# Kernel tuning notes

Measured on AMD Instinct MI355X. Metric: run time of the kernel, lower is better.

## Reference

```python
import jax, jax.numpy as jnp
import numpy as np

# NaiveMatryoshkaLinear(dim=4096, hidden_dim=4096, heads=[8,8,16], bias=False)
# head_dim = 4096 // 32 = 128
# input_dims  (cumsum heads * head_dim) = [1024, 2048, 4096]
# output_dims (heads * head_dim)        = [1024, 1024, 2048]
INPUT_DIMS = (1024, 2048, 4096)
OUTPUT_DIMS = (1024, 1024, 2048)


def setup_inputs() -> dict:
    key = jax.random.key(0)
    kx, k0, k1, k2 = jax.random.split(key, 4)
    x = jax.random.normal(kx, (4, 4096, 4096), dtype=jnp.float32)
    # torch nn.Linear weight layout: (out_features, in_features), kaiming-uniform-ish init
    def init_w(k, out_d, in_d):
        bound = 1.0 / np.sqrt(in_d)
        return jax.random.uniform(k, (out_d, in_d), dtype=jnp.float32, minval=-bound, maxval=bound)
    W0 = init_w(k0, OUTPUT_DIMS[0], INPUT_DIMS[0])
    W1 = init_w(k1, OUTPUT_DIMS[1], INPUT_DIMS[1])
    W2 = init_w(k2, OUTPUT_DIMS[2], INPUT_DIMS[2])
    return {"x": x, "W0": W0, "W1": W1, "W2": W2}


def reference(x, W0, W1, W2):
    # Block-triangular matryoshka linear: each head i projects the prefix
    # x[..., :input_dims[i]] with its own weight, outputs are concatenated.
    y0 = jnp.einsum('bsd,od->bso', x[..., :INPUT_DIMS[0]], W0)
    y1 = jnp.einsum('bsd,od->bso', x[..., :INPUT_DIMS[1]], W1)
    y2 = jnp.einsum('bsd,od->bso', x[..., :INPUT_DIMS[2]], W2)
    return jnp.concatenate([y0, y1, y2], axis=-1)  # [4, 4096, 4096]
```

## Files before the change

### kernel.cpp

```cpp
#include <hip/hip_runtime.h>
#include <hip/hip_bf16.h>


typedef short bf16x8 __attribute__((ext_vector_type(8)));
typedef float f32x4 __attribute__((ext_vector_type(4)));

__device__ __forceinline__ ushort f2bf(float f) {
  union { float f; unsigned u; } c; c.f = f;
  unsigned u = c.u;
  unsigned r = u + 0x7fffu + ((u >> 16) & 1u);
  return (ushort)(r >> 16);
}

__global__ void cvt_all_bf16(const float* __restrict__ x,
                             const float* __restrict__ W0,
                             const float* __restrict__ W1,
                             const float* __restrict__ W2,
                             ushort* __restrict__ dst) {
  const int X4  = 16777216;
  const int E0  = X4 + 262144;
  const int E1  = E0 + 524288;
  const int E2  = E1 + 2097152;
  int i = blockIdx.x * blockDim.x + threadIdx.x;
  int stride = gridDim.x * blockDim.x;
  ushort4* out4 = (ushort4*)dst;
  for (int j = i; j < E2; j += stride) {
    const float4* src;
    if (j < X4)      src = (const float4*)x  + j;
    else if (j < E0) src = (const float4*)W0 + (j - X4);
    else if (j < E1) src = (const float4*)W1 + (j - E0);
    else             src = (const float4*)W2 + (j - E1);
    float4 v = *src;
    ushort4 o;
    o.x = f2bf(v.x); o.y = f2bf(v.y); o.z = f2bf(v.z); o.w = f2bf(v.w);
    out4[j] = o;
  }
}

__device__ __forceinline__ void gload16(const ushort* g, const ushort* l) {
  __builtin_amdgcn_global_load_lds(
      (const __attribute__((address_space(1))) void*)g,
      (__attribute__((address_space(3))) void*)l, 16, 0, 0);
}

#define TILE_E 8192

#define MF(av, bv, mi, ni) \
  acc[mi][ni] = __builtin_amdgcn_mfma_f32_16x16x32_bf16(av, bv, acc[mi][ni], 0, 0, 0)

__global__ __launch_bounds__(512, 2) void matry_gemm(
    const ushort* __restrict__ xbf,
    const ushort* __restrict__ w0,
    const ushort* __restrict__ w1,
    const ushort* __restrict__ w2,
    float* __restrict__ out) {
  __shared__ __align__(16) ushort sA[4][TILE_E];
  __shared__ __align__(16) ushort sB[4][TILE_E];

  const int bid = blockIdx.x;
  const int rt = bid & 63;
  const int ct = bid >> 6;

  int K; const ushort* W; int nl0;
  if (ct < 4)      { K = 1024; W = w0; nl0 = ct * 256; }
  else if (ct < 8) { K = 2048; W = w1; nl0 = (ct - 4) * 256; }
  else             { K = 4096; W = w2; nl0 = (ct - 8) * 256; }
  const int NT = K >> 5;
  const int m0 = rt * 256;
  const int n0 = ct * 256;

  const int tid  = threadIdx.x;
  const int wid  = tid >> 6;
  const int lane = tid & 63;
  const int wm = wid >> 2;
  const int wn = wid & 3;
  const int fr = lane & 15;
  const int swz_e = (((lane >> 4) ^ ((lane >> 1) & 3)) << 3);

  const int srow = tid >> 2;
  const int scol = (((tid & 3) ^ ((tid >> 3) & 3)) << 3);
  const ushort* Asrc0 = xbf + (size_t)(m0 + srow) * 4096 + scol;
  const ushort* Asrc1 = Asrc0 + (size_t)128 * 4096;
  const ushort* Bsrc0 = W + (size_t)(nl0 + srow) * K + scol;
  const ushort* Bsrc1 = Bsrc0 + (size_t)128 * K;
  const int d0 = tid * 8;
  const int d1 = 4096 + tid * 8;

  f32x4 acc[8][4];
#pragma unroll
  for (int mi = 0; mi < 8; ++mi)
#pragma unroll
    for (int ni = 0; ni < 4; ++ni)
      acc[mi][ni] = (f32x4){0.f, 0.f, 0.f, 0.f};

#pragma unroll
  for (int pt = 0; pt < 3; ++pt) {
    const int ks = pt * 32;
    gload16(Asrc0 + ks, &sA[pt][d0]);
    gload16(Asrc1 + ks, &sA[pt][d1]);
    gload16(Bsrc0 + ks, &sB[pt][d0]);
    gload16(Bsrc1 + ks, &sB[pt][d1]);
  }
  asm volatile("s_waitcnt vmcnt(8)" ::: "memory");
  __builtin_amdgcn_s_barrier();

  for (int t = 0; t < NT; ++t) {
    const int b = t & 3;
    const ushort* pa = &sA[b][(wm * 128 + fr) * 32 + swz_e];
    const ushort* pb = &sB[b][(wn * 64 + fr) * 32 + swz_e];
    const int ts = (t + 3 < NT) ? (t + 3) : (NT - 1);
    const int ks = ts << 5;
    const int bs = (t + 3) & 3;

    bf16x8 a0 = *(const bf16x8*)(pa);
    bf16x8 a1 = *(const bf16x8*)(pa + 512);
    bf16x8 a2 = *(const bf16x8*)(pa + 1024);
    bf16x8 a3 = *(const bf16x8*)(pa + 1536);
    bf16x8 b0 = *(const bf16x8*)(pb);
    bf16x8 b1 = *(const bf16x8*)(pb + 512);
    bf16x8 b2 = *(const bf16x8*)(pb + 1024);
    bf16x8 b3 = *(const bf16x8*)(pb + 1536);
    gload16(Asrc0 + ks, &sA[bs][d0]);
    gload16(Asrc1 + ks, &sA[bs][d1]);
    __builtin_amdgcn_s_barrier();
    asm volatile("s_waitcnt lgkmcnt(0)" ::: "memory");
    __builtin_amdgcn_s_setprio(1);
    MF(a0, b0, 0, 0); MF(a0, b1, 0, 1); MF(a0, b2, 0, 2); MF(a0, b3, 0, 3);
    MF(a1, b0, 1, 0); MF(a1, b1, 1, 1); MF(a1, b2, 1, 2); MF(a1, b3, 1, 3);
    MF(a2, b0, 2, 0); MF(a2, b1, 2, 1); MF(a2, b2, 2, 2); MF(a2, b3, 2, 3);
    MF(a3, b0, 3, 0); MF(a3, b1, 3, 1); MF(a3, b2, 3, 2); MF(a3, b3, 3, 3);
    __builtin_amdgcn_s_setprio(0);
    __builtin_amdgcn_s_barrier();

    bf16x8 a4 = *(const bf16x8*)(pa + 2048);
    bf16x8 a5 = *(const bf16x8*)(pa + 2560);
    bf16x8 a6 = *(const bf16x8*)(pa + 3072);
    bf16x8 a7 = *(const bf16x8*)(pa + 3584);
    gload16(Bsrc0 + ks, &sB[bs][d0]);
    gload16(Bsrc1 + ks, &sB[bs][d1]);
    __builtin_amdgcn_s_barrier();
    asm volatile("s_waitcnt lgkmcnt(0)" ::: "memory");
    __builtin_amdgcn_s_setprio(1);
    MF(a4, b0, 4, 0); MF(a4, b1, 4, 1); MF(a4, b2, 4, 2); MF(a4, b3, 4, 3);
    MF(a5, b0, 5, 0); MF(a5, b1, 5, 1); MF(a5, b2, 5, 2); MF(a5, b3, 5, 3);
    MF(a6, b0, 6, 0); MF(a6, b1, 6, 1); MF(a6, b2, 6, 2); MF(a6, b3, 6, 3);
    MF(a7, b0, 7, 0); MF(a7, b1, 7, 1); MF(a7, b2, 7, 2); MF(a7, b3, 7, 3);
    __builtin_amdgcn_s_setprio(0);
    asm volatile("s_waitcnt vmcnt(8)" ::: "memory");
    __builtin_amdgcn_s_barrier();
  }

  const int rq = (lane >> 4) * 4;
#pragma unroll
  for (int mi = 0; mi < 8; ++mi) {
#pragma unroll
    for (int ni = 0; ni < 4; ++ni) {
      const int n = n0 + wn * 64 + ni * 16 + fr;
#pragma unroll
      for (int r = 0; r < 4; ++r) {
        const int m = m0 + wm * 128 + mi * 16 + rq + r;
        out[(size_t)m * 4096 + n] = acc[mi][ni][r];
      }
    }
  }
}

__global__ void naive_kernel(const float* __restrict__ x,
                             const float* __restrict__ W0,
                             const float* __restrict__ W1,
                             const float* __restrict__ W2,
                             float* __restrict__ out) {
  long idx = (long)blockIdx.x * 256 + threadIdx.x;
  int n = (int)(idx & 4095);
  long m = idx >> 12;
  int K; const float* W; int nl;
  if (n < 1024)      { K = 1024; W = W0; nl = n; }
  else if (n < 2048) { K = 2048; W = W1; nl = n - 1024; }
  else               { K = 4096; W = W2; nl = n - 2048; }
  const float* xr = x + m * 4096;
  const float* wr = W + (long)nl * K;
  float s = 0.f;
  for (int k = 0; k < K; ++k) s += xr[k] * wr[k];
  out[idx] = s;
}

extern "C" void kernel_launch(void* const* d_in, const int* in_sizes, int n_in,
                              void* d_out, int out_size, void* d_ws,
                              size_t ws_size, hipStream_t stream) {
  const float* x  = (const float*)d_in[0];
  const float* W0 = (const float*)d_in[1];
  const float* W1 = (const float*)d_in[2];
  const float* W2 = (const float*)d_in[3];
  float* out = (float*)d_out;

  const size_t xN  = (size_t)16384 * 4096;
  const size_t w0N = (size_t)1024 * 1024;
  const size_t w1N = (size_t)1024 * 2048;
  const size_t w2N = (size_t)2048 * 4096;
  const size_t need = (xN + w0N + w1N + w2N) * sizeof(ushort);

  if (ws_size >= need) {
    ushort* xbf = (ushort*)d_ws;
    ushort* w0b = xbf + xN;
    ushort* w1b = w0b + w0N;
    ushort* w2b = w1b + w1N;
    cvt_all_bf16<<<4096, 256, 0, stream>>>(x, W0, W1, W2, xbf);
    matry_gemm<<<1024, 512, 0, stream>>>(xbf, w0b, w1b, w2b, out);
  } else {
    naive_kernel<<<(int)((xN + 255) / 256), 256, 0, stream>>>(x, W0, W1, W2, out);
  }
}
```

Before: 478.5 us.

## Restructure GEMM main loop to double-buffered 64-wide K steps with half-tile buffers

Replaces the four-deep ring of 32-wide K tiles with two double-buffered halves (sA0/sA1, sB0/sB1), so each loop iteration processes 64 of K in four MFMA phases. Prefetch distance drops from three tiles to the next 64-wide step, and register reuse is tightened by recycling the a/b fragment variables. The intent is less loop overhead and bookkeeping per MFMA while keeping LDS usage the same. In exchange the prefetch is shallower, which may expose more global-load latency, and the vmcnt accounting changes.

New measurement: 563.9 us. 1.18x slower.

```diff
diff --git a/kernel.cpp b/kernel.cpp
--- a/kernel.cpp
+++ b/kernel.cpp
@@ -43,10 +43,20 @@
       (__attribute__((address_space(3))) void*)l, 16, 0, 0);
 }
 
-#define TILE_E 8192
-
 #define MF(av, bv, mi, ni) \
   acc[mi][ni] = __builtin_amdgcn_mfma_f32_16x16x32_bf16(av, bv, acc[mi][ni], 0, 0, 0)
+
+#define MFQ0(A0, A1, A2, A3) \
+  MF(A0, b0, 0, 0); MF(A0, b1, 0, 1); MF(A0, b2, 0, 2); MF(A0, b3, 0, 3); \
+  MF(A1, b0, 1, 0); MF(A1, b1, 1, 1); MF(A1, b2, 1, 2); MF(A1, b3, 1, 3); \
+  MF(A2, b0, 2, 0); MF(A2, b1, 2, 1); MF(A2, b2, 2, 2); MF(A2, b3, 2, 3); \
+  MF(A3, b0, 3, 0); MF(A3, b1, 3, 1); MF(A3, b2, 3, 2); MF(A3, b3, 3, 3)
+
+#define MFQ1(A0, A1, A2, A3) \
+  MF(A0, b0, 4, 0); MF(A0, b1, 4, 1); MF(A0, b2, 4, 2); MF(A0, b3, 4, 3); \
+  MF(A1, b0, 5, 0); MF(A1, b1, 5, 1); MF(A1, b2, 5, 2); MF(A1, b3, 5, 3); \
+  MF(A2, b0, 6, 0); MF(A2, b1, 6, 1); MF(A2, b2, 6, 2); MF(A2, b3, 6, 3); \
+  MF(A3, b0, 7, 0); MF(A3, b1, 7, 1); MF(A3, b2, 7, 2); MF(A3, b3, 7, 3)
 
 __global__ __launch_bounds__(512, 2) void matry_gemm(
     const ushort* __restrict__ xbf,
@@ -54,8 +64,10 @@
     const ushort* __restrict__ w1,
     const ushort* __restrict__ w2,
     float* __restrict__ out) {
-  __shared__ __align__(16) ushort sA[4][TILE_E];
-  __shared__ __align__(16) ushort sB[4][TILE_E];
+  __shared__ __align__(16) ushort sA0[2][8192];
+  __shared__ __align__(16) ushort sA1[2][8192];
+  __shared__ __align__(16) ushort sB0[2][8192];
+  __shared__ __align__(16) ushort sB1[2][8192];
 
   const int bid = blockIdx.x;
   const int rt = bid & 63;
@@ -65,7 +77,7 @@
   if (ct < 4)      { K = 1024; W = w0; nl0 = ct * 256; }
   else if (ct < 8) { K = 2048; W = w1; nl0 = (ct - 4) * 256; }
   else             { K = 4096; W = w2; nl0 = (ct - 8) * 256; }
-  const int NT = K >> 5;
+  const int NT = K >> 6;
   const int m0 = rt * 256;
   const int n0 = ct * 256;
 
@@ -77,14 +89,16 @@
   const int fr = lane & 15;
   const int swz_e = (((lane >> 4) ^ ((lane >> 1) & 3)) << 3);
 
+  const int aoff = (wm * 128 + fr) * 32 + swz_e;
+  const int boff = (wn * 64 + fr) * 32 + swz_e;
+
   const int srow = tid >> 2;
   const int scol = (((tid & 3) ^ ((tid >> 3) & 3)) << 3);
-  const ushort* Asrc0 = xbf + (size_t)(m0 + srow) * 4096 + scol;
-  const ushort* Asrc1 = Asrc0 + (size_t)128 * 4096;
-  const ushort* Bsrc0 = W + (size_t)(nl0 + srow) * K + scol;
-  const ushort* Bsrc1 = Bsrc0 + (size_t)128 * K;
-  const int d0 = tid * 8;
-  const int d1 = 4096 + tid * 8;
+  const ushort* Ag = xbf + (size_t)(m0 + srow) * 4096 + scol;
+  const ushort* Bg = W + (size_t)(nl0 + srow) * K + scol;
+  const size_t Ac1 = (size_t)128 * 4096;
+  const size_t Bc1 = (size_t)128 * K;
+  const int dst0 = tid * 8, dst1 = 4096 + tid * 8;
 
   f32x4 acc[8][4];
 #pragma unroll
@@ -93,60 +107,88 @@
     for (int ni = 0; ni < 4; ++ni)
       acc[mi][ni] = (f32x4){0.f, 0.f, 0.f, 0.f};
 
-#pragma unroll
-  for (int pt = 0; pt < 3; ++pt) {
-    const int ks = pt * 32;
-    gload16(Asrc0 + ks, &sA[pt][d0]);
-    gload16(Asrc1 + ks, &sA[pt][d1]);
-    gload16(Bsrc0 + ks, &sB[pt][d0]);
-    gload16(Bsrc1 + ks, &sB[pt][d1]);
-  }
-  asm volatile("s_waitcnt vmcnt(8)" ::: "memory");
+  gload16(Ag, &sA0[0][dst0]);
+  gload16(Ag + Ac1, &sA0[0][dst1]);
+  gload16(Bg, &sB0[0][dst0]);
+  gload16(Bg + Bc1, &sB0[0][dst1]);
+  gload16(Ag + 32, &sA1[0][dst0]);
+  gload16(Ag + Ac1 + 32, &sA1[0][dst1]);
+  gload16(Bg + 32, &sB1[0][dst0]);
+  gload16(Bg + Bc1 + 32, &sB1[0][dst1]);
+  asm volatile("s_waitcnt vmcnt(4)" ::: "memory");
   __builtin_amdgcn_s_barrier();
 
   for (int t = 0; t < NT; ++t) {
-    const int b = t & 3;
-    const ushort* pa = &sA[b][(wm * 128 + fr) * 32 + swz_e];
-    const ushort* pb = &sB[b][(wn * 64 + fr) * 32 + swz_e];
-    const int ts = (t + 3 < NT) ? (t + 3) : (NT - 1);
-    const int ks = ts << 5;
-    const int bs = (t + 3) & 3;
-
-    bf16x8 a0 = *(const bf16x8*)(pa);
-    bf16x8 a1 = *(const bf16x8*)(pa + 512);
-    bf16x8 a2 = *(const bf16x8*)(pa + 1024);
-    bf16x8 a3 = *(const bf16x8*)(pa + 1536);
-    bf16x8 b0 = *(const bf16x8*)(pb);
-    bf16x8 b1 = *(const bf16x8*)(pb + 512);
-    bf16x8 b2 = *(const bf16x8*)(pb + 1024);
-    bf16x8 b3 = *(const bf16x8*)(pb + 1536);
-    gload16(Asrc0 + ks, &sA[bs][d0]);
-    gload16(Asrc1 + ks, &sA[bs][d1]);
-    __builtin_amdgcn_s_barrier();
-    asm volatile("s_waitcnt lgkmcnt(0)" ::: "memory");
-    __builtin_amdgcn_s_setprio(1);
-    MF(a0, b0, 0, 0); MF(a0, b1, 0, 1); MF(a0, b2, 0, 2); MF(a0, b3, 0, 3);
-    MF(a1, b0, 1, 0); MF(a1, b1, 1, 1); MF(a1, b2, 1, 2); MF(a1, b3, 1, 3);
-    MF(a2, b0, 2, 0); MF(a2, b1, 2, 1); MF(a2, b2, 2, 2); MF(a2, b3, 2, 3);
-    MF(a3, b0, 3, 0); MF(a3, b1, 3, 1); MF(a3, b2, 3, 2); MF(a3, b3, 3, 3);
-    __builtin_amdgcn_s_setprio(0);
-    __builtin_amdgcn_s_barrier();
-
-    bf16x8 a4 = *(const bf16x8*)(pa + 2048);
-    bf16x8 a5 = *(const bf16x8*)(pa + 2560);
-    bf16x8 a6 = *(const bf16x8*)(pa + 3072);
-    bf16x8 a7 = *(const bf16x8*)(pa + 3584);
-    gload16(Bsrc0 + ks, &sB[bs][d0]);
-    gload16(Bsrc1 + ks, &sB[bs][d1]);
-    __builtin_amdgcn_s_barrier();
-    asm volatile("s_waitcnt lgkmcnt(0)" ::: "memory");
-    __builtin_amdgcn_s_setprio(1);
-    MF(a4, b0, 4, 0); MF(a4, b1, 4, 1); MF(a4, b2, 4, 2); MF(a4, b3, 4, 3);
-    MF(a5, b0, 5, 0); MF(a5, b1, 5, 1); MF(a5, b2, 5, 2); MF(a5, b3, 5, 3);
-    MF(a6, b0, 6, 0); MF(a6, b1, 6, 1); MF(a6, b2, 6, 2); MF(a6, b3, 6, 3);
-    MF(a7, b0, 7, 0); MF(a7, b1, 7, 1); MF(a7, b2, 7, 2); MF(a7, b3, 7, 3);
-    __builtin_amdgcn_s_setprio(0);
-    asm volatile("s_waitcnt vmcnt(8)" ::: "memory");
+    const int cur = t & 1, nb = cur ^ 1;
+    const ushort* a0p = &sA0[cur][aoff];
+    const ushort* a1p = &sA1[cur][aoff];
+    const ushort* b0p = &sB0[cur][boff];
+    const ushort* b1p = &sB1[cur][boff];
+    const int tk = (t + 1 < NT) ? (t + 1) : (NT - 1);
+    const size_t kg = (size_t)tk * 64;
+
+    bf16x8 a0, a1, a2, a3, b0, b1, b2, b3;
+
+    a0 = *(const bf16x8*)(a0p);
+    a1 = *(const bf16x8*)(a0p + 512);
+    a2 = *(const bf16x8*)(a0p + 1024);
+    a3 = *(const bf16x8*)(a0p + 1536);
+    b0 = *(const bf16x8*)(b0p);
+    b1 = *(const bf16x8*)(b0p + 512);
+    b2 = *(const bf16x8*)(b0p + 1024);
+    b3 = *(const bf16x8*)(b0p + 1536);
+    gload16(Ag + kg, &sA0[nb][dst0]);
+    gload16(Ag + Ac1 + kg, &sA0[nb][dst1]);
+    __builtin_amdgcn_s_barrier();
+    asm volatile("s_waitcnt lgkmcnt(0)" ::: "memory");
+    __builtin_amdgcn_s_setprio(1);
+    MFQ0(a0, a1, a2, a3);
+    __builtin_amdgcn_s_setprio(0);
+    __builtin_amdgcn_s_barrier();
+
+    a0 = *(const bf16x8*)(a0p + 2048);
+    a1 = *(const bf16x8*)(a0p + 2560);
+    a2 = *(const bf16x8*)(a0p + 3072);
+    a3 = *(const bf16x8*)(a0p + 3584);
+    gload16(Bg + kg, &sB0[nb][dst0]);
+    gload16(Bg + Bc1 + kg, &sB0[nb][dst1]);
+    __builtin_amdgcn_s_barrier();
+    asm volatile("s_waitcnt lgkmcnt(0)" ::: "memory");
+    __builtin_amdgcn_s_setprio(1);
+    MFQ1(a0, a1, a2, a3);
+    __builtin_amdgcn_s_setprio(0);
+    asm volatile("s_waitcnt vmcnt(4)" ::: "memory");
+    __builtin_amdgcn_s_barrier();
+
+    a0 = *(const bf16x8*)(a1p);
+    a1 = *(const bf16x8*)(a1p + 512);
+    a2 = *(const bf16x8*)(a1p + 1024);
+    a3 = *(const bf16x8*)(a1p + 1536);
+    b0 = *(const bf16x8*)(b1p);
+    b1 = *(const bf16x8*)(b1p + 512);
+    b2 = *(const bf16x8*)(b1p + 1024);
+    b3 = *(const bf16x8*)(b1p + 1536);
+    gload16(Ag + kg + 32, &sA1[nb][dst0]);
+    gload16(Ag + Ac1 + kg + 32, &sA1[nb][dst1]);
+    __builtin_amdgcn_s_barrier();
+    asm volatile("s_waitcnt lgkmcnt(0)" ::: "memory");
+    __builtin_amdgcn_s_setprio(1);
+    MFQ0(a0, a1, a2, a3);
+    __builtin_amdgcn_s_setprio(0);
+    __builtin_amdgcn_s_barrier();
+
+    a0 = *(const bf16x8*)(a1p + 2048);
+    a1 = *(const bf16x8*)(a1p + 2560);
+    a2 = *(const bf16x8*)(a1p + 3072);
+    a3 = *(const bf16x8*)(a1p + 3584);
+    gload16(Bg + kg + 32, &sB1[nb][dst0]);
+    gload16(Bg + Bc1 + kg + 32, &sB1[nb][dst1]);
+    __builtin_amdgcn_s_barrier();
+    asm volatile("s_waitcnt lgkmcnt(0)" ::: "memory");
+    __builtin_amdgcn_s_setprio(1);
+    MFQ1(a0, a1, a2, a3);
+    __builtin_amdgcn_s_setprio(0);
+    asm volatile("s_waitcnt vmcnt(4)" ::: "memory");
     __builtin_amdgcn_s_barrier();
   }
 
```
